# Kernel tuning notes

Measured on AMD Instinct MI355X. Metric: run time of the kernel, lower is better.

Reference implementation:

```python
import jax, jax.numpy as jnp
import numpy as np

D = 1024       # d_model
S = 32         # n_slots
EMA = 0.05     # slot_ema (alpha)
RSCALE = 1.0   # read_logit_scale
LN_EPS = 1e-5


def setup_inputs() -> dict:
    key = jax.random.key(0)
    ks = jax.random.split(key, 6)
    B, T = 2, 2048
    h = jax.random.normal(ks[0], (B, T, D), jnp.float32)
    # init_batched_memory_state: small random slots
    state0 = jax.random.normal(ks[1], (B, S, D), jnp.float32) * 0.01
    # xavier_uniform for (out=D, in=D) Linear weights, zero bias
    bound = float(np.sqrt(6.0 / (D + D)))
    Wq = jax.random.uniform(ks[2], (D, D), jnp.float32, -bound, bound)
    Wv = jax.random.uniform(ks[3], (D, D), jnp.float32, -bound, bound)
    bq = jnp.zeros((D,), jnp.float32)
    bv = jnp.zeros((D,), jnp.float32)
    ln_gamma = jnp.ones((D,), jnp.float32)
    ln_beta = jnp.zeros((D,), jnp.float32)
    return {"h": h, "state0": state0, "ln_gamma": ln_gamma, "ln_beta": ln_beta,
            "Wq": Wq, "bq": bq, "Wv": Wv, "bv": bv, "chunk_size": 128}


def _layer_norm(x, gamma, beta):
    mu = jnp.mean(x, axis=-1, keepdims=True)
    var = jnp.mean(jnp.square(x - mu), axis=-1, keepdims=True)
    return (x - mu) * jax.lax.rsqrt(var + LN_EPS) * gamma + beta


def reference(h, state0, ln_gamma, ln_beta, Wq, bq, Wv, bv, chunk_size):
    """write_parallel (soft-routed EMA prefix-scan write) followed by
    read_parallel (per-token softmax slot attention). Returns (ctx, final_state)."""
    B, T, d = h.shape
    alpha = EMA
    a = 1.0 - alpha
    h_norm = _layer_norm(h, ln_gamma, ln_beta)                  # (B,T,d)
    v = h_norm @ Wv.T + bv                                      # value_proj
    q = h_norm @ Wq.T + bq                                      # query_proj
    scale = RSCALE * d ** (-0.5)
    # routing weights from queries vs initial state (breaks seq dependency)
    scores = jnp.einsum('btd,bsd->bts', q, state0) * scale       # (B,T,S)
    w = jax.nn.softmax(scores, axis=-1)
    u = alpha * w[..., None] * v[:, :, None, :]                  # (B,T,S,d)

    n_chunks = T // chunk_size
    Cn = chunk_size
    u_chunks = u.reshape(B, n_chunks, Cn, S, d).transpose(1, 0, 2, 3, 4)
    t_idx = jnp.arange(Cn, dtype=h.dtype)
    decay = a ** t_idx                                           # (Cn,)
    inv_decay = 1.0 / jnp.clip(decay, 1e-30)
    t1_decay = a ** (t_idx + 1.0)

    def step(state, u_c):  # state (B,S,d), u_c (B,Cn,S,d)
        cs = jnp.cumsum(u_c * inv_decay[None, :, None, None], axis=1)
        chunk_states = (decay[None, :, None, None] * cs
                        + t1_decay[None, :, None, None] * state[:, None])
        return chunk_states[:, -1], chunk_states

    final_state, states = jax.lax.scan(step, state0, u_chunks)
    states = states.transpose(1, 0, 2, 3, 4).reshape(B, T, S, d)  # (B,T,S,d)

    # read_parallel: softmax slot attention per token against its own state
    scores_r = jnp.einsum('btd,btsd->bts', q, states) * scale
    attn = jax.nn.softmax(scores_r, axis=-1)
    ctx = jnp.einsum('bts,btsd->btd', attn, states)               # (B,T,d)
    return ctx, final_state
```

## Files before the change

### kernel.cpp

```cpp
#include <hip/hip_runtime.h>

#define Bn 2
#define Tn 2048
#define Dn 1024
#define Sn 32
#define CH 64
#define NCH 32
#define ALPHA 0.05f
#define Adec 0.95f
#define SCALE 0.03125f

typedef __attribute__((ext_vector_type(8))) __bf16 bf16x8;
typedef __attribute__((ext_vector_type(4))) __bf16 bf16x4;
typedef __attribute__((ext_vector_type(4))) float f32x4;

__device__ __forceinline__ void async_copy16(const void* g, void* l) {
  __builtin_amdgcn_global_load_lds(
      (const __attribute__((address_space(1))) unsigned int*)g,
      (__attribute__((address_space(3))) unsigned int*)l, 16, 0, 0);
}

__global__ void flag_k(const unsigned short* __restrict__ g, int* __restrict__ flag) {
  *flag = (g[0] == 0x3F80u) ? 1 : 0;
}

#define W8 (Dn * Dn / 8)
#define S8 (Bn * Sn * Dn / 8)
__global__ __launch_bounds__(256) void conv_k(
    const void* __restrict__ Wq, const void* __restrict__ Wv,
    const void* __restrict__ s0, const int* __restrict__ flag,
    __bf16* __restrict__ Wqb, __bf16* __restrict__ Wvb, __bf16* __restrict__ s0b) {
  bool isb = (*flag != 0);
  int g = blockIdx.x * 256 + threadIdx.x;
  const void* src; __bf16* dst; int off;
  if (g < W8)            { src = Wq; dst = Wqb; off = g; }
  else if (g < 2 * W8)   { src = Wv; dst = Wvb; off = g - W8; }
  else                   { src = s0; dst = s0b; off = g - 2 * W8; }
  if (isb) {
    *(bf16x8*)&dst[(size_t)off * 8] = ((const bf16x8*)src)[off];
  } else {
    const float* s = (const float*)src + (size_t)off * 8;
    f32x4 a = *(const f32x4*)s, b = *(const f32x4*)(s + 4);
    bf16x8 t;
    t[0] = (__bf16)a[0]; t[1] = (__bf16)a[1]; t[2] = (__bf16)a[2]; t[3] = (__bf16)a[3];
    t[4] = (__bf16)b[0]; t[5] = (__bf16)b[1]; t[6] = (__bf16)b[2]; t[7] = (__bf16)b[3];
    *(bf16x8*)&dst[(size_t)off * 8] = t;
  }
}

__global__ __launch_bounds__(256) void ln_k(const void* __restrict__ hp,
    const void* __restrict__ gp, const void* __restrict__ bp,
    const int* __restrict__ flag, __bf16* __restrict__ hn) {
  int row = blockIdx.x;
  int tid = threadIdx.x;
  bool isb = (*flag != 0);
  float x0, x1, x2, x3;
  if (isb) {
    const __bf16* x = (const __bf16*)hp + (size_t)row * Dn;
    bf16x4 xv = *(const bf16x4*)&x[tid * 4];
    x0 = (float)xv[0]; x1 = (float)xv[1]; x2 = (float)xv[2]; x3 = (float)xv[3];
  } else {
    const float* x = (const float*)hp + (size_t)row * Dn;
    f32x4 xv = *(const f32x4*)&x[tid * 4];
    x0 = xv[0]; x1 = xv[1]; x2 = xv[2]; x3 = xv[3];
  }
  float s  = x0 + x1 + x2 + x3;
  float s2 = x0*x0 + x1*x1 + x2*x2 + x3*x3;
  #pragma unroll
  for (int m = 32; m >= 1; m >>= 1) { s += __shfl_xor(s, m); s2 += __shfl_xor(s2, m); }
  __shared__ float red[8];
  int wave = tid >> 6, lane = tid & 63;
  if (lane == 0) { red[wave] = s; red[4 + wave] = s2; }
  __syncthreads();
  s  = red[0] + red[1] + red[2] + red[3];
  s2 = red[4] + red[5] + red[6] + red[7];
  float mu  = s * (1.0f / Dn);
  float var = s2 * (1.0f / Dn) - mu * mu;
  float rs  = rsqrtf(var + 1e-5f);
  float g0, g1, g2, g3, be0, be1, be2, be3;
  if (isb) {
    bf16x4 gv = *(const bf16x4*)&((const __bf16*)gp)[tid * 4];
    bf16x4 bv = *(const bf16x4*)&((const __bf16*)bp)[tid * 4];
    g0 = (float)gv[0]; g1 = (float)gv[1]; g2 = (float)gv[2]; g3 = (float)gv[3];
    be0 = (float)bv[0]; be1 = (float)bv[1]; be2 = (float)bv[2]; be3 = (float)bv[3];
  } else {
    f32x4 gv = *(const f32x4*)&((const float*)gp)[tid * 4];
    f32x4 bv = *(const f32x4*)&((const float*)bp)[tid * 4];
    g0 = gv[0]; g1 = gv[1]; g2 = gv[2]; g3 = gv[3];
    be0 = bv[0]; be1 = bv[1]; be2 = bv[2]; be3 = bv[3];
  }
  bf16x4 o;
  o[0] = (__bf16)((x0 - mu) * rs * g0 + be0);
  o[1] = (__bf16)((x1 - mu) * rs * g1 + be1);
  o[2] = (__bf16)((x2 - mu) * rs * g2 + be2);
  o[3] = (__bf16)((x3 - mu) * rs * g3 + be3);
  *(bf16x4*)&hn[(size_t)row * Dn + tid * 4] = o;
}

__global__ __launch_bounds__(256) void gemm_qv_k(
    const __bf16* __restrict__ A,
    const __bf16* __restrict__ Wqb, const void* __restrict__ bqp,
    const __bf16* __restrict__ Wvb, const void* __restrict__ bvp,
    const int* __restrict__ flag,
    __bf16* __restrict__ Qo, __bf16* __restrict__ Vo) {
  const int K = Dn, N = Dn;
  bool isb = (*flag != 0);
  int mt = blockIdx.x & 31;
  int ng = blockIdx.x >> 5;
  const __bf16* W; const void* biasp; __bf16* O; int nt;
  if (ng < 8) { W = Wqb; biasp = bqp; O = Qo; nt = ng; }
  else        { W = Wvb; biasp = bvp; O = Vo; nt = ng - 8; }
  int m0 = mt * 128, n0 = nt * 128;
  __shared__ alignas(16) __bf16 lA[128 * 64];
  __shared__ alignas(16) __bf16 lB[128 * 64];
  int tid = threadIdx.x, lane = tid & 63, wave = tid >> 6;
  int wm = (wave >> 1) * 64, wn = (wave & 1) * 64;
  int lm = lane & 15, q8 = (lane >> 4) * 8;
  f32x4 zero4 = {0.f, 0.f, 0.f, 0.f};
  f32x4 acc[4][4];
  #pragma unroll
  for (int i = 0; i < 4; ++i)
    #pragma unroll
    for (int j = 0; j < 4; ++j) acc[i][j] = zero4;

  for (int k0 = 0; k0 < K; k0 += 64) {
    __syncthreads();
    #pragma unroll
    for (int r = 0; r < 4; ++r) {
      int idx = r * 256 + tid;
      int row = idx >> 3, c8 = (idx & 7) * 8;
      async_copy16(&A[(size_t)(m0 + row) * K + k0 + c8], &lA[idx * 8]);
      async_copy16(&W[(size_t)(n0 + row) * K + k0 + c8], &lB[idx * 8]);
    }
    __syncthreads();
    #pragma unroll
    for (int kk = 0; kk < 64; kk += 32) {
      bf16x8 af[4], bfr[4];
      #pragma unroll
      for (int i = 0; i < 4; ++i) {
        af[i]  = *(const bf16x8*)&lA[(wm + i * 16 + lm) * 64 + kk + q8];
        bfr[i] = *(const bf16x8*)&lB[(wn + i * 16 + lm) * 64 + kk + q8];
      }
      #pragma unroll
      for (int i = 0; i < 4; ++i)
        #pragma unroll
        for (int j = 0; j < 4; ++j)
          acc[i][j] = __builtin_amdgcn_mfma_f32_16x16x32_bf16(af[i], bfr[j], acc[i][j], 0, 0, 0);
    }
  }
  int r4 = (lane >> 4) * 4;
  #pragma unroll
  for (int j = 0; j < 4; ++j) {
    int colN = n0 + wn + j * 16 + lm;
    float bb = isb ? (float)((const __bf16*)biasp)[colN] : ((const float*)biasp)[colN];
    #pragma unroll
    for (int i = 0; i < 4; ++i) {
      int row0 = m0 + wm + i * 16 + r4;
      #pragma unroll
      for (int r = 0; r < 4; ++r)
        O[(size_t)(row0 + r) * N + colN] = (__bf16)(acc[i][j][r] + bb);
    }
  }
}

#define SP 33
__global__ __launch_bounds__(256) void router_k(const __bf16* __restrict__ qb,
    const __bf16* __restrict__ s0b, float* __restrict__ wbuf) {
  int tokBase = blockIdx.x * 64;
  int b = tokBase >> 11;
  const __bf16* S = s0b + (size_t)b * Sn * Dn;
  __shared__ alignas(16) __bf16 lQ[64 * 64];
  __shared__ alignas(16) __bf16 lS[Sn * 64];
  __shared__ float fSc[64 * SP];
  int tid = threadIdx.x, lane = tid & 63, wave = tid >> 6;
  int lm = lane & 15, q8 = (lane >> 4) * 8;
  f32x4 zero4 = {0.f, 0.f, 0.f, 0.f};
  f32x4 acc[2]; acc[0] = zero4; acc[1] = zero4;

  for (int k0 = 0; k0 < Dn; k0 += 64) {
    __syncthreads();
    #pragma unroll
    for (int r = 0; r < 2; ++r) {
      int idx = r * 256 + tid;
      async_copy16(&qb[(size_t)(tokBase + (idx >> 3)) * Dn + k0 + (idx & 7) * 8], &lQ[idx * 8]);
    }
    async_copy16(&S[(size_t)(tid >> 3) * Dn + k0 + (tid & 7) * 8], &lS[tid * 8]);
    __syncthreads();
    #pragma unroll
    for (int kk = 0; kk < 64; kk += 32) {
      bf16x8 af = *(const bf16x8*)&lQ[(wave * 16 + lm) * 64 + kk + q8];
      #pragma unroll
      for (int j = 0; j < 2; ++j) {
        bf16x8 bb = *(const bf16x8*)&lS[(j * 16 + lm) * 64 + kk + q8];
        acc[j] = __builtin_amdgcn_mfma_f32_16x16x32_bf16(af, bb, acc[j], 0, 0, 0);
      }
    }
  }
  int r4 = (lane >> 4) * 4;
  #pragma unroll
  for (int j = 0; j < 2; ++j)
    #pragma unroll
    for (int r = 0; r < 4; ++r)
      fSc[(wave * 16 + r4 + r) * SP + j * 16 + lm] = acc[j][r];
  __syncthreads();
  if (tid < 64) {
    int t = tid;
    float mx = -1e30f;
    #pragma unroll
    for (int s = 0; s < Sn; ++s) mx = fmaxf(mx, fSc[t * SP + s]);
    float sum = 0.f;
    float ex[Sn];
    #pragma unroll
    for (int s = 0; s < Sn; ++s) { ex[s] = __expf(fSc[t * SP + s] * SCALE - mx * SCALE); sum += ex[s]; }
    float inv = 1.f / sum;
    #pragma unroll
    for (int s = 0; s < Sn; ++s)
      wbuf[(size_t)(tokBase + t) * Sn + s] = ex[s] * inv;
  }
}

__global__ __launch_bounds__(256) void contrib_k(const __bf16* __restrict__ v,
    const float* __restrict__ wbuf, float* __restrict__ contrib) {
  int blk = blockIdx.x;
  int bc = blk >> 2, dq = blk & 3;
  int b = bc >> 5, c = bc & 31;
  int tokBase = b * Tn + c * CH;
  int d0 = dq * 256;
  __shared__ alignas(16) float coef[CH * Sn];
  __shared__ float dp[CH];
  int tid = threadIdx.x;
  if (tid < CH) dp[tid] = powf(Adec, (float)(CH - 1 - tid));
  __syncthreads();
  for (int i = tid; i < CH * Sn; i += 256) {
    int j = i >> 5;
    coef[i] = ALPHA * dp[j] * wbuf[(size_t)tokBase * Sn + i];
  }
  __syncthreads();
  int st = tid >> 6;
  int dg = tid & 63;
  int d4 = d0 + dg * 4;
  int sb = st * 8;
  f32x4 zero4 = {0.f, 0.f, 0.f, 0.f};
  f32x4 acc[8];
  #pragma unroll
  for (int i = 0; i < 8; ++i) acc[i] = zero4;
  for (int j = 0; j < CH; ++j) {
    bf16x4 vv = *(const bf16x4*)&v[(size_t)(tokBase + j) * Dn + d4];
    f32x4 vf = {(float)vv[0], (float)vv[1], (float)vv[2], (float)vv[3]};
    f32x4 c0 = *(const f32x4*)&coef[j * Sn + sb];
    f32x4 c1 = *(const f32x4*)&coef[j * Sn + sb + 4];
    acc[0] += vf * c0[0]; acc[1] += vf * c0[1]; acc[2] += vf * c0[2]; acc[3] += vf * c0[3];
    acc[4] += vf * c1[0]; acc[5] += vf * c1[1]; acc[6] += vf * c1[2]; acc[7] += vf * c1[3];
  }
  float* outp = contrib + (size_t)bc * Sn * Dn;
  #pragma unroll
  for (int i = 0; i < 8; ++i)
    *(f32x4*)&outp[(size_t)(sb + i) * Dn + d4] = acc[i];
}

__global__ __launch_bounds__(256) void scan_k(const void* __restrict__ s0p,
    const float* __restrict__ contrib, const int* __restrict__ flag,
    float* __restrict__ S0buf, void* __restrict__ outp) {
  int idx = blockIdx.x * 256 + threadIdx.x;
  bool isb = (*flag != 0);
  int b = idx >> 15, sd = idx & 32767;
  float val = isb ? (float)((const __bf16*)s0p)[idx] : ((const float*)s0p)[idx];
  const float aC = powf(Adec, (float)CH);
  #pragma unroll 8
  for (int c = 0; c < NCH; ++c) {
    size_t off = ((size_t)(b * NCH + c) << 15) + sd;
    S0buf[off] = val;
    val = aC * val + contrib[off];
  }
  size_t fsbase = (size_t)Bn * Tn * Dn;
  if (isb) ((__bf16*)outp)[fsbase + idx] = (__bf16)val;
  else     ((float*)outp)[fsbase + idx] = val;
}

#define QVP 65
__global__ __launch_bounds__(256) void attn_k(
    const __bf16* __restrict__ q, const __bf16* __restrict__ v,
    const float* __restrict__ wbuf, const float* __restrict__ S0buf,
    float* __restrict__ Pbuf, float* __restrict__ A2buf) {
  int bc = blockIdx.x;
  int b = bc >> 5, c = bc & 31;
  int tokBase = b * Tn + c * CH;
  const float* S0c = S0buf + (size_t)bc * Sn * Dn;

  __shared__ alignas(16) __bf16 lQ[CH * 64];
  __shared__ alignas(16) __bf16 lV[CH * 64];
  __shared__ alignas(16) __bf16 lS[Sn * 64];
  __shared__ float fQV[CH * QVP];
  __shared__ float fQS[CH * SP];
  __shared__ float fW[CH * SP];
  __shared__ float fA[CH * SP];
  __shared__ float dp[CH];

  int tid = threadIdx.x, lane = tid & 63, wave = tid >> 6;
  int lm = lane & 15, q8 = (lane >> 4) * 8;
  f32x4 zero4 = {0.f, 0.f, 0.f, 0.f};
  f32x4 aQV[4], aQS[2];
  #pragma unroll
  for (int i = 0; i < 4; ++i) aQV[i] = zero4;
  aQS[0] = zero4; aQS[1] = zero4;

  for (int k0 = 0; k0 < Dn; k0 += 64) {
    __syncthreads();
    #pragma unroll
    for (int r = 0; r < 2; ++r) {
      int idx = r * 256 + tid;
      int row = idx >> 3, c8 = (idx & 7) * 8;
      async_copy16(&q[(size_t)(tokBase + row) * Dn + k0 + c8], &lQ[idx * 8]);
      async_copy16(&v[(size_t)(tokBase + row) * Dn + k0 + c8], &lV[idx * 8]);
    }
    {
      int s = tid >> 3, c8 = (tid & 7) * 8;
      const float* src = S0c + (size_t)s * Dn + k0 + c8;
      f32x4 a0 = *(const f32x4*)&src[0];
      f32x4 a1 = *(const f32x4*)&src[4];
      bf16x8 t8;
      t8[0] = (__bf16)a0[0]; t8[1] = (__bf16)a0[1]; t8[2] = (__bf16)a0[2]; t8[3] = (__bf16)a0[3];
      t8[4] = (__bf16)a1[0]; t8[5] = (__bf16)a1[1]; t8[6] = (__bf16)a1[2]; t8[7] = (__bf16)a1[3];
      *(bf16x8*)&lS[s * 64 + c8] = t8;
    }
    __syncthreads();
    #pragma unroll
    for (int kk = 0; kk < 64; kk += 32) {
      bf16x8 af = *(const bf16x8*)&lQ[(wave * 16 + lm) * 64 + kk + q8];
      #pragma unroll
      for (int j = 0; j < 4; ++j) {
        bf16x8 bb = *(const bf16x8*)&lV[(j * 16 + lm) * 64 + kk + q8];
        aQV[j] = __builtin_amdgcn_mfma_f32_16x16x32_bf16(af, bb, aQV[j], 0, 0, 0);
      }
      #pragma unroll
      for (int j = 0; j < 2; ++j) {
        bf16x8 bb = *(const bf16x8*)&lS[(j * 16 + lm) * 64 + kk + q8];
        aQS[j] = __builtin_amdgcn_mfma_f32_16x16x32_bf16(af, bb, aQS[j], 0, 0, 0);
      }
    }
  }
  int r4 = (lane >> 4) * 4;
  #pragma unroll
  for (int j = 0; j < 4; ++j)
    #pragma unroll
    for (int r = 0; r < 4; ++r)
      fQV[(wave * 16 + r4 + r) * QVP + j * 16 + lm] = aQV[j][r];
  #pragma unroll
  for (int j = 0; j < 2; ++j)
    #pragma unroll
    for (int r = 0; r < 4; ++r)
      fQS[(wave * 16 + r4 + r) * SP + j * 16 + lm] = aQS[j][r];
  for (int i = tid; i < CH * Sn; i += 256) {
    int j = i >> 5, s = i & 31;
    fW[j * SP + s] = wbuf[(size_t)tokBase * Sn + i];
  }
  if (tid < CH) dp[tid] = powf(Adec, (float)tid);
  __syncthreads();

  {
    int t = tid >> 2, sg = (tid & 3) * 8;
    float sc[8];
    float aQ = Adec * dp[t];
    #pragma unroll
    for (int e = 0; e < 8; ++e) sc[e] = aQ * fQS[t * SP + sg + e];
    for (int j = 0; j <= t; ++j) {
      float m = ALPHA * dp[t - j] * fQV[t * QVP + j];
      #pragma unroll
      for (int e = 0; e < 8; ++e) sc[e] += m * fW[j * SP + sg + e];
    }
    #pragma unroll
    for (int e = 0; e < 8; ++e) fA[t * SP + sg + e] = sc[e] * SCALE;
  }
  __syncthreads();
  if (tid < CH) {
    int t = tid;
    float mx = -1e30f;
    for (int s = 0; s < Sn; ++s) mx = fmaxf(mx, fA[t * SP + s]);
    float sum = 0.f;
    for (int s = 0; s < Sn; ++s) { float e = __expf(fA[t * SP + s] - mx); fA[t * SP + s] = e; sum += e; }
    float inv = 1.f / sum;
    float a1 = Adec * dp[t];
    for (int s = 0; s < Sn; ++s) {
      float at = fA[t * SP + s] * inv;
      fA[t * SP + s] = at;
      A2buf[(size_t)bc * CH * Sn + t * Sn + s] = a1 * at;
    }
  }
  __syncthreads();
  for (int it = 0; it < 16; ++it) {
    int e = it * 256 + tid;
    int t = e >> 6, j = e & 63;
    float p = 0.f;
    if (j <= t) {
      float aw = 0.f;
      #pragma unroll
      for (int s = 0; s < Sn; ++s) aw += fA[t * SP + s] * fW[j * SP + s];
      p = ALPHA * dp[t - j] * aw;
    }
    Pbuf[(size_t)bc * CH * CH + e] = p;
  }
}

__global__ __launch_bounds__(256) void ctx_k(const __bf16* __restrict__ v,
    const float* __restrict__ S0buf, const float* __restrict__ Pbuf,
    const float* __restrict__ A2buf, const int* __restrict__ flag,
    void* __restrict__ ctxp) {
  int blk = blockIdx.x;
  int bc = blk >> 3, dt = blk & 7;
  int b = bc >> 5, c = bc & 31;
  int tokBase = b * Tn + c * CH;
  int d0 = dt * 128;
  bool isb = (*flag != 0);
  __shared__ alignas(16) float lP[CH * CH];
  __shared__ alignas(16) float lA2[CH * Sn];
  __shared__ alignas(16) __bf16 lV[CH * 128];
  __shared__ alignas(16) float lS[Sn * 128];
  int tid = threadIdx.x;
  {
    const f32x4* src = (const f32x4*)(Pbuf + (size_t)bc * CH * CH);
    f32x4* dst = (f32x4*)lP;
    for (int i = tid; i < CH * CH / 4; i += 256) dst[i] = src[i];
    const f32x4* src2 = (const f32x4*)(A2buf + (size_t)bc * CH * Sn);
    f32x4* dst2 = (f32x4*)lA2;
    for (int i = tid; i < CH * Sn / 4; i += 256) dst2[i] = src2[i];
    for (int i = tid; i < CH * 128 / 8; i += 256) {
      int j = i >> 4, dd = (i & 15) * 8;
      *(bf16x8*)&lV[j * 128 + dd] = *(const bf16x8*)&v[(size_t)(tokBase + j) * Dn + d0 + dd];
    }
    for (int i = tid; i < Sn * 128 / 4; i += 256) {
      int s = i >> 5, dd = (i & 31) * 4;
      *(f32x4*)&lS[s * 128 + dd] = *(const f32x4*)&S0buf[((size_t)bc * Sn + s) * Dn + d0 + dd];
    }
  }
  __syncthreads();
  int tt = tid >> 5, dg = tid & 31;
  int t0 = tt * 8, d4 = dg * 4;
  f32x4 zero4 = {0.f, 0.f, 0.f, 0.f};
  f32x4 acc[8];
  #pragma unroll
  for (int i = 0; i < 8; ++i) acc[i] = zero4;
  for (int j = 0; j < CH; ++j) {
    bf16x4 vv = *(const bf16x4*)&lV[j * 128 + d4];
    f32x4 vf = {(float)vv[0], (float)vv[1], (float)vv[2], (float)vv[3]};
    #pragma unroll
    for (int i = 0; i < 8; ++i) acc[i] += vf * lP[(t0 + i) * CH + j];
  }
  for (int s = 0; s < Sn; ++s) {
    f32x4 sv = *(const f32x4*)&lS[s * 128 + d4];
    #pragma unroll
    for (int i = 0; i < 8; ++i) acc[i] += sv * lA2[(t0 + i) * Sn + s];
  }
  if (isb) {
    __bf16* ctx = (__bf16*)ctxp;
    #pragma unroll
    for (int i = 0; i < 8; ++i) {
      bf16x4 o;
      o[0] = (__bf16)acc[i][0]; o[1] = (__bf16)acc[i][1];
      o[2] = (__bf16)acc[i][2]; o[3] = (__bf16)acc[i][3];
      *(bf16x4*)&ctx[(size_t)(tokBase + t0 + i) * Dn + d0 + d4] = o;
    }
  } else {
    float* ctx = (float*)ctxp;
    #pragma unroll
    for (int i = 0; i < 8; ++i)
      *(f32x4*)&ctx[(size_t)(tokBase + t0 + i) * Dn + d0 + d4] = acc[i];
  }
}

extern "C" void kernel_launch(void* const* d_in, const int* in_sizes, int n_in,
                              void* d_out, int out_size, void* d_ws, size_t ws_size,
                              hipStream_t stream) {
  (void)in_sizes; (void)n_in; (void)out_size; (void)ws_size;
  const void* h      = d_in[0];
  const void* state0 = d_in[1];
  const void* gam    = d_in[2];
  const void* bet    = d_in[3];
  const void* Wq     = d_in[4];
  const void* bq     = d_in[5];
  const void* Wv     = d_in[6];
  const void* bv     = d_in[7];

  char* ws = (char*)d_ws;
  __bf16* hn      = (__bf16*)(ws);
  __bf16* qb      = (__bf16*)(ws + (8u << 20));
  __bf16* vb      = (__bf16*)(ws + (16u << 20));
  float*  wbuf    = (float*)(ws + (24u << 20));
  float*  contrib = (float*)(ws + (25u << 20));
  float*  S0buf   = (float*)(ws + (34u << 20));
  float*  Pbuf    = (float*)(ws + (43u << 20));
  float*  A2buf   = (float*)(ws + (45u << 20));
  int*    flag    = (int*)(ws + (46u << 20));
  __bf16* Wqb     = (__bf16*)(ws + (47u << 20));
  __bf16* Wvb     = (__bf16*)(ws + (49u << 20));
  __bf16* s0b     = (__bf16*)(ws + (51u << 20));

  flag_k<<<1, 1, 0, stream>>>((const unsigned short*)gam, flag);
  conv_k<<<(2 * W8 + S8) / 256, 256, 0, stream>>>(Wq, Wv, state0, flag, Wqb, Wvb, s0b);
  ln_k<<<Bn * Tn, 256, 0, stream>>>(h, gam, bet, flag, hn);
  gemm_qv_k<<<512, 256, 0, stream>>>(hn, Wqb, bq, Wvb, bv, flag, qb, vb);
  router_k<<<Bn * Tn / 64, 256, 0, stream>>>(qb, s0b, wbuf);
  contrib_k<<<Bn * NCH * 4, 256, 0, stream>>>(vb, wbuf, contrib);
  scan_k<<<Bn * Sn * Dn / 256, 256, 0, stream>>>(state0, contrib, flag, S0buf, d_out);
  attn_k<<<Bn * NCH, 256, 0, stream>>>(qb, vb, wbuf, S0buf, Pbuf, A2buf);
  ctx_k<<<Bn * NCH * 8, 256, 0, stream>>>(vb, S0buf, Pbuf, A2buf, flag, d_out);
}
```

Measured before the change: 196.7 us.

## Move chunk attention scores to MFMA, store chunk states in bf16, drop flag kernel

The per-chunk attention kernel now computes its causal score matrix and its P = attn·W^T products with bf16 MFMA instructions instead of scalar loops over shared-memory floats, with softmax done via lane shuffles. Chunk-start states are written as bf16 so they can be async-copied into LDS and read at half the bandwidth in both consumers. The separate flag kernel is removed and each kernel checks the dtype itself, and the context kernel's inner loops are unrolled by four with vector loads. This cuts scalar FLOPs, traffic and one launch, at the cost of lower precision in the state and attention products.

```diff
diff --git a/kernel.cpp b/kernel.cpp
--- a/kernel.cpp
+++ b/kernel.cpp
@@ -20,17 +20,17 @@
       (__attribute__((address_space(3))) unsigned int*)l, 16, 0, 0);
 }
 
-__global__ void flag_k(const unsigned short* __restrict__ g, int* __restrict__ flag) {
-  *flag = (g[0] == 0x3F80u) ? 1 : 0;
+__device__ __forceinline__ bool is_bf16(const void* gam) {
+  return ((const unsigned short*)gam)[0] == 0x3F80u;
 }
 
 #define W8 (Dn * Dn / 8)
 #define S8 (Bn * Sn * Dn / 8)
 __global__ __launch_bounds__(256) void conv_k(
     const void* __restrict__ Wq, const void* __restrict__ Wv,
-    const void* __restrict__ s0, const int* __restrict__ flag,
+    const void* __restrict__ s0, const void* __restrict__ gam,
     __bf16* __restrict__ Wqb, __bf16* __restrict__ Wvb, __bf16* __restrict__ s0b) {
-  bool isb = (*flag != 0);
+  bool isb = is_bf16(gam);
   int g = blockIdx.x * 256 + threadIdx.x;
   const void* src; __bf16* dst; int off;
   if (g < W8)            { src = Wq; dst = Wqb; off = g; }
@@ -50,10 +50,10 @@
 
 __global__ __launch_bounds__(256) void ln_k(const void* __restrict__ hp,
     const void* __restrict__ gp, const void* __restrict__ bp,
-    const int* __restrict__ flag, __bf16* __restrict__ hn) {
+    __bf16* __restrict__ hn) {
   int row = blockIdx.x;
   int tid = threadIdx.x;
-  bool isb = (*flag != 0);
+  bool isb = is_bf16(gp);
   float x0, x1, x2, x3;
   if (isb) {
     const __bf16* x = (const __bf16*)hp + (size_t)row * Dn;
@@ -101,10 +101,10 @@
     const __bf16* __restrict__ A,
     const __bf16* __restrict__ Wqb, const void* __restrict__ bqp,
     const __bf16* __restrict__ Wvb, const void* __restrict__ bvp,
-    const int* __restrict__ flag,
+    const void* __restrict__ gam,
     __bf16* __restrict__ Qo, __bf16* __restrict__ Vo) {
   const int K = Dn, N = Dn;
-  bool isb = (*flag != 0);
+  bool isb = is_bf16(gam);
   int mt = blockIdx.x & 31;
   int ng = blockIdx.x >> 5;
   const __bf16* W; const void* biasp; __bf16* O; int nt;
@@ -259,17 +259,17 @@
 }
 
 __global__ __launch_bounds__(256) void scan_k(const void* __restrict__ s0p,
-    const float* __restrict__ contrib, const int* __restrict__ flag,
-    float* __restrict__ S0buf, void* __restrict__ outp) {
+    const float* __restrict__ contrib, const void* __restrict__ gam,
+    __bf16* __restrict__ S0b, void* __restrict__ outp) {
   int idx = blockIdx.x * 256 + threadIdx.x;
-  bool isb = (*flag != 0);
+  bool isb = is_bf16(gam);
   int b = idx >> 15, sd = idx & 32767;
   float val = isb ? (float)((const __bf16*)s0p)[idx] : ((const float*)s0p)[idx];
   const float aC = powf(Adec, (float)CH);
   #pragma unroll 8
   for (int c = 0; c < NCH; ++c) {
     size_t off = ((size_t)(b * NCH + c) << 15) + sd;
-    S0buf[off] = val;
+    S0b[off] = (__bf16)val;
     val = aC * val + contrib[off];
   }
   size_t fsbase = (size_t)Bn * Tn * Dn;
@@ -277,32 +277,40 @@
   else     ((float*)outp)[fsbase + idx] = val;
 }
 
-#define QVP 65
 __global__ __launch_bounds__(256) void attn_k(
     const __bf16* __restrict__ q, const __bf16* __restrict__ v,
-    const float* __restrict__ wbuf, const float* __restrict__ S0buf,
+    const float* __restrict__ wbuf, const __bf16* __restrict__ S0b,
     float* __restrict__ Pbuf, float* __restrict__ A2buf) {
   int bc = blockIdx.x;
   int b = bc >> 5, c = bc & 31;
   int tokBase = b * Tn + c * CH;
-  const float* S0c = S0buf + (size_t)bc * Sn * Dn;
+  const __bf16* S0c = S0b + (size_t)bc * Sn * Dn;
 
   __shared__ alignas(16) __bf16 lQ[CH * 64];
   __shared__ alignas(16) __bf16 lV[CH * 64];
   __shared__ alignas(16) __bf16 lS[Sn * 64];
-  __shared__ float fQV[CH * QVP];
-  __shared__ float fQS[CH * SP];
-  __shared__ float fW[CH * SP];
-  __shared__ float fA[CH * SP];
-  __shared__ float dp[CH];
+  __shared__ alignas(16) __bf16 lM[CH * 72];
+  __shared__ alignas(16) __bf16 lW[CH * 40];
+  __shared__ alignas(16) __bf16 lWt[Sn * 72];
+  __shared__ alignas(16) __bf16 lAt[CH * 40];
+  __shared__ float dp[CH + 1];
 
   int tid = threadIdx.x, lane = tid & 63, wave = tid >> 6;
   int lm = lane & 15, q8 = (lane >> 4) * 8;
+  int r4 = (lane >> 4) * 4;
   f32x4 zero4 = {0.f, 0.f, 0.f, 0.f};
   f32x4 aQV[4], aQS[2];
   #pragma unroll
   for (int i = 0; i < 4; ++i) aQV[i] = zero4;
   aQS[0] = zero4; aQS[1] = zero4;
+
+  for (int i = tid; i < CH * Sn; i += 256) {
+    int j = i >> 5, s = i & 31;
+    __bf16 wb = (__bf16)wbuf[(size_t)tokBase * Sn + i];
+    lW[j * 40 + s] = wb;
+    lWt[s * 72 + j] = wb;
+  }
+  if (tid < CH + 1) dp[tid] = powf(Adec, (float)tid);
 
   for (int k0 = 0; k0 < Dn; k0 += 64) {
     __syncthreads();
@@ -313,16 +321,7 @@
       async_copy16(&q[(size_t)(tokBase + row) * Dn + k0 + c8], &lQ[idx * 8]);
       async_copy16(&v[(size_t)(tokBase + row) * Dn + k0 + c8], &lV[idx * 8]);
     }
-    {
-      int s = tid >> 3, c8 = (tid & 7) * 8;
-      const float* src = S0c + (size_t)s * Dn + k0 + c8;
-      f32x4 a0 = *(const f32x4*)&src[0];
-      f32x4 a1 = *(const f32x4*)&src[4];
-      bf16x8 t8;
-      t8[0] = (__bf16)a0[0]; t8[1] = (__bf16)a0[1]; t8[2] = (__bf16)a0[2]; t8[3] = (__bf16)a0[3];
-      t8[4] = (__bf16)a1[0]; t8[5] = (__bf16)a1[1]; t8[6] = (__bf16)a1[2]; t8[7] = (__bf16)a1[3];
-      *(bf16x8*)&lS[s * 64 + c8] = t8;
-    }
+    async_copy16(&S0c[(size_t)(tid >> 3) * Dn + k0 + (tid & 7) * 8], &lS[tid * 8]);
     __syncthreads();
     #pragma unroll
     for (int kk = 0; kk < 64; kk += 32) {
@@ -339,82 +338,75 @@
       }
     }
   }
-  int r4 = (lane >> 4) * 4;
-  #pragma unroll
-  for (int j = 0; j < 4; ++j)
-    #pragma unroll
-    for (int r = 0; r < 4; ++r)
-      fQV[(wave * 16 + r4 + r) * QVP + j * 16 + lm] = aQV[j][r];
-  #pragma unroll
-  for (int j = 0; j < 2; ++j)
-    #pragma unroll
-    for (int r = 0; r < 4; ++r)
-      fQS[(wave * 16 + r4 + r) * SP + j * 16 + lm] = aQS[j][r];
-  for (int i = tid; i < CH * Sn; i += 256) {
-    int j = i >> 5, s = i & 31;
-    fW[j * SP + s] = wbuf[(size_t)tokBase * Sn + i];
-  }
-  if (tid < CH) dp[tid] = powf(Adec, (float)tid);
-  __syncthreads();
-
-  {
-    int t = tid >> 2, sg = (tid & 3) * 8;
-    float sc[8];
-    float aQ = Adec * dp[t];
-    #pragma unroll
-    for (int e = 0; e < 8; ++e) sc[e] = aQ * fQS[t * SP + sg + e];
-    for (int j = 0; j <= t; ++j) {
-      float m = ALPHA * dp[t - j] * fQV[t * QVP + j];
-      #pragma unroll
-      for (int e = 0; e < 8; ++e) sc[e] += m * fW[j * SP + sg + e];
-    }
-    #pragma unroll
-    for (int e = 0; e < 8; ++e) fA[t * SP + sg + e] = sc[e] * SCALE;
-  }
-  __syncthreads();
-  if (tid < CH) {
-    int t = tid;
-    float mx = -1e30f;
-    for (int s = 0; s < Sn; ++s) mx = fmaxf(mx, fA[t * SP + s]);
-    float sum = 0.f;
-    for (int s = 0; s < Sn; ++s) { float e = __expf(fA[t * SP + s] - mx); fA[t * SP + s] = e; sum += e; }
-    float inv = 1.f / sum;
-    float a1 = Adec * dp[t];
-    for (int s = 0; s < Sn; ++s) {
-      float at = fA[t * SP + s] * inv;
-      fA[t * SP + s] = at;
-      A2buf[(size_t)bc * CH * Sn + t * Sn + s] = a1 * at;
-    }
-  }
-  __syncthreads();
-  for (int it = 0; it < 16; ++it) {
-    int e = it * 256 + tid;
-    int t = e >> 6, j = e & 63;
-    float p = 0.f;
-    if (j <= t) {
-      float aw = 0.f;
-      #pragma unroll
-      for (int s = 0; s < Sn; ++s) aw += fA[t * SP + s] * fW[j * SP + s];
-      p = ALPHA * dp[t - j] * aw;
-    }
-    Pbuf[(size_t)bc * CH * CH + e] = p;
+
+  #pragma unroll
+  for (int jt = 0; jt < 4; ++jt)
+    #pragma unroll
+    for (int r = 0; r < 4; ++r) {
+      int t = wave * 16 + r4 + r, j = jt * 16 + lm;
+      float f = (j <= t) ? ALPHA * dp[t - j] : 0.0f;
+      lM[t * 72 + j] = (__bf16)(aQV[jt][r] * f);
+    }
+
+  f32x4 sc[2]; sc[0] = zero4; sc[1] = zero4;
+  #pragma unroll
+  for (int kt = 0; kt < 2; ++kt) {
+    bf16x8 am = *(const bf16x8*)&lM[(wave * 16 + lm) * 72 + kt * 32 + q8];
+    #pragma unroll
+    for (int st = 0; st < 2; ++st) {
+      bf16x8 bb = *(const bf16x8*)&lWt[(st * 16 + lm) * 72 + kt * 32 + q8];
+      sc[st] = __builtin_amdgcn_mfma_f32_16x16x32_bf16(am, bb, sc[st], 0, 0, 0);
+    }
+  }
+  float at0[4], at1[4];
+  #pragma unroll
+  for (int r = 0; r < 4; ++r) {
+    int t = wave * 16 + r4 + r;
+    float aQ = dp[t - wave * 16 + 1 + wave * 16];
+    float s0v = SCALE * (aQ * aQS[0][r] + sc[0][r]);
+    float s1v = SCALE * (aQ * aQS[1][r] + sc[1][r]);
+    float mx = fmaxf(s0v, s1v);
+    #pragma unroll
+    for (int m = 8; m >= 1; m >>= 1) mx = fmaxf(mx, __shfl_xor(mx, m));
+    float e0 = __expf(s0v - mx), e1 = __expf(s1v - mx);
+    float su = e0 + e1;
+    #pragma unroll
+    for (int m = 8; m >= 1; m >>= 1) su += __shfl_xor(su, m);
+    float inv = 1.f / su;
+    at0[r] = e0 * inv; at1[r] = e1 * inv;
+    A2buf[(size_t)bc * CH * Sn + t * Sn + lm]      = aQ * at0[r];
+    A2buf[(size_t)bc * CH * Sn + t * Sn + 16 + lm] = aQ * at1[r];
+    lAt[t * 40 + lm]      = (__bf16)at0[r];
+    lAt[t * 40 + 16 + lm] = (__bf16)at1[r];
+  }
+  bf16x8 aa = *(const bf16x8*)&lAt[(wave * 16 + lm) * 40 + q8];
+  #pragma unroll
+  for (int jt = 0; jt < 4; ++jt) {
+    bf16x8 bb = *(const bf16x8*)&lW[(jt * 16 + lm) * 40 + q8];
+    f32x4 pj = __builtin_amdgcn_mfma_f32_16x16x32_bf16(aa, bb, zero4, 0, 0, 0);
+    #pragma unroll
+    for (int r = 0; r < 4; ++r) {
+      int t = wave * 16 + r4 + r, j = jt * 16 + lm;
+      float val = (j <= t) ? ALPHA * dp[t - j] * pj[r] : 0.0f;
+      Pbuf[(size_t)bc * CH * CH + t * CH + j] = val;
+    }
   }
 }
 
 __global__ __launch_bounds__(256) void ctx_k(const __bf16* __restrict__ v,
-    const float* __restrict__ S0buf, const float* __restrict__ Pbuf,
-    const float* __restrict__ A2buf, const int* __restrict__ flag,
+    const __bf16* __restrict__ S0b, const float* __restrict__ Pbuf,
+    const float* __restrict__ A2buf, const void* __restrict__ gam,
     void* __restrict__ ctxp) {
   int blk = blockIdx.x;
   int bc = blk >> 3, dt = blk & 7;
   int b = bc >> 5, c = bc & 31;
   int tokBase = b * Tn + c * CH;
   int d0 = dt * 128;
-  bool isb = (*flag != 0);
+  bool isb = is_bf16(gam);
   __shared__ alignas(16) float lP[CH * CH];
   __shared__ alignas(16) float lA2[CH * Sn];
   __shared__ alignas(16) __bf16 lV[CH * 128];
-  __shared__ alignas(16) float lS[Sn * 128];
+  __shared__ alignas(16) __bf16 lS[Sn * 128];
   int tid = threadIdx.x;
   {
     const f32x4* src = (const f32x4*)(Pbuf + (size_t)bc * CH * CH);
@@ -427,9 +419,9 @@
       int j = i >> 4, dd = (i & 15) * 8;
       *(bf16x8*)&lV[j * 128 + dd] = *(const bf16x8*)&v[(size_t)(tokBase + j) * Dn + d0 + dd];
     }
-    for (int i = tid; i < Sn * 128 / 4; i += 256) {
-      int s = i >> 5, dd = (i & 31) * 4;
-      *(f32x4*)&lS[s * 128 + dd] = *(const f32x4*)&S0buf[((size_t)bc * Sn + s) * Dn + d0 + dd];
+    for (int i = tid; i < Sn * 128 / 8; i += 256) {
+      int s = i >> 4, dd = (i & 15) * 8;
+      *(bf16x8*)&lS[s * 128 + dd] = *(const bf16x8*)&S0b[((size_t)bc * Sn + s) * Dn + d0 + dd];
     }
   }
   __syncthreads();
@@ -439,16 +431,33 @@
   f32x4 acc[8];
   #pragma unroll
   for (int i = 0; i < 8; ++i) acc[i] = zero4;
-  for (int j = 0; j < CH; ++j) {
-    bf16x4 vv = *(const bf16x4*)&lV[j * 128 + d4];
-    f32x4 vf = {(float)vv[0], (float)vv[1], (float)vv[2], (float)vv[3]};
-    #pragma unroll
-    for (int i = 0; i < 8; ++i) acc[i] += vf * lP[(t0 + i) * CH + j];
-  }
-  for (int s = 0; s < Sn; ++s) {
-    f32x4 sv = *(const f32x4*)&lS[s * 128 + d4];
-    #pragma unroll
-    for (int i = 0; i < 8; ++i) acc[i] += sv * lA2[(t0 + i) * Sn + s];
+  for (int j4 = 0; j4 < CH; j4 += 4) {
+    f32x4 vf[4];
+    #pragma unroll
+    for (int k = 0; k < 4; ++k) {
+      bf16x4 vv = *(const bf16x4*)&lV[(j4 + k) * 128 + d4];
+      vf[k] = f32x4{(float)vv[0], (float)vv[1], (float)vv[2], (float)vv[3]};
+    }
+    #pragma unroll
+    for (int i = 0; i < 8; ++i) {
+      f32x4 pr = *(const f32x4*)&lP[(t0 + i) * CH + j4];
+      acc[i] += vf[0] * pr[0]; acc[i] += vf[1] * pr[1];
+      acc[i] += vf[2] * pr[2]; acc[i] += vf[3] * pr[3];
+    }
+  }
+  for (int s4 = 0; s4 < Sn; s4 += 4) {
+    f32x4 sf[4];
+    #pragma unroll
+    for (int k = 0; k < 4; ++k) {
+      bf16x4 sv = *(const bf16x4*)&lS[(s4 + k) * 128 + d4];
+      sf[k] = f32x4{(float)sv[0], (float)sv[1], (float)sv[2], (float)sv[3]};
+    }
+    #pragma unroll
+    for (int i = 0; i < 8; ++i) {
+      f32x4 ar = *(const f32x4*)&lA2[(t0 + i) * Sn + s4];
+      acc[i] += sf[0] * ar[0]; acc[i] += sf[1] * ar[1];
+      acc[i] += sf[2] * ar[2]; acc[i] += sf[3] * ar[3];
+    }
   }
   if (isb) {
     __bf16* ctx = (__bf16*)ctxp;
@@ -486,21 +495,19 @@
   __bf16* vb      = (__bf16*)(ws + (16u << 20));
   float*  wbuf    = (float*)(ws + (24u << 20));
   float*  contrib = (float*)(ws + (25u << 20));
-  float*  S0buf   = (float*)(ws + (34u << 20));
+  __bf16* S0b     = (__bf16*)(ws + (34u << 20));
   float*  Pbuf    = (float*)(ws + (43u << 20));
   float*  A2buf   = (float*)(ws + (45u << 20));
-  int*    flag    = (int*)(ws + (46u << 20));
   __bf16* Wqb     = (__bf16*)(ws + (47u << 20));
   __bf16* Wvb     = (__bf16*)(ws + (49u << 20));
   __bf16* s0b     = (__bf16*)(ws + (51u << 20));
 
-  flag_k<<<1, 1, 0, stream>>>((const unsigned short*)gam, flag);
-  conv_k<<<(2 * W8 + S8) / 256, 256, 0, stream>>>(Wq, Wv, state0, flag, Wqb, Wvb, s0b);
-  ln_k<<<Bn * Tn, 256, 0, stream>>>(h, gam, bet, flag, hn);
-  gemm_qv_k<<<512, 256, 0, stream>>>(hn, Wqb, bq, Wvb, bv, flag, qb, vb);
+  conv_k<<<(2 * W8 + S8) / 256, 256, 0, stream>>>(Wq, Wv, state0, gam, Wqb, Wvb, s0b);
+  ln_k<<<Bn * Tn, 256, 0, stream>>>(h, gam, bet, hn);
+  gemm_qv_k<<<512, 256, 0, stream>>>(hn, Wqb, bq, Wvb, bv, gam, qb, vb);
   router_k<<<Bn * Tn / 64, 256, 0, stream>>>(qb, s0b, wbuf);
   contrib_k<<<Bn * NCH * 4, 256, 0, stream>>>(vb, wbuf, contrib);
-  scan_k<<<Bn * Sn * Dn / 256, 256, 0, stream>>>(state0, contrib, flag, S0buf, d_out);
-  attn_k<<<Bn * NCH, 256, 0, stream>>>(qb, vb, wbuf, S0buf, Pbuf, A2buf);
-  ctx_k<<<Bn * NCH * 8, 256, 0, stream>>>(vb, S0buf, Pbuf, A2buf, flag, d_out);
-}
+  scan_k<<<Bn * Sn * Dn / 256, 256, 0, stream>>>(state0, contrib, gam, S0b, d_out);
+  attn_k<<<Bn * NCH, 256, 0, stream>>>(qb, vb, wbuf, S0b, Pbuf, A2buf);
+  ctx_k<<<Bn * NCH * 8, 256, 0, stream>>>(vb, S0b, Pbuf, A2buf, gam, d_out);
+}
```

After: 184.1 us. 1.07x faster.
